# Kernel tuning notes

Hardware: AMD Instinct MI355X
Metric: run time of the kernel (lower is better)

The kernel has to match this reference:

```python
import jax, jax.numpy as jnp
import numpy as np

B, S, E, H = 4, 512, 512, 8
DH = E // H
HID = max(16, E // 4)  # sr_ratio=4
ALPHA = 0.1
EPS_SAFE = 0.05  # eps=1e-6 clamped to [0.05, 0.8]


def _xavier(k, shape):
    fan_out, fan_in = shape[0], shape[1]
    lim = (6.0 / (fan_in + fan_out)) ** 0.5
    return jax.random.uniform(k, shape, minval=-lim, maxval=lim, dtype=jnp.float32)


def setup_inputs() -> dict:
    key = jax.random.key(0)
    ks = jax.random.split(key, 8)
    return {
        "x": jax.random.normal(ks[0], (B, S, E), dtype=jnp.float32),
        "wq": _xavier(ks[1], (E, E)), "bq": jnp.zeros((E,), jnp.float32),
        "wk": _xavier(ks[2], (E, E)), "bk": jnp.zeros((E,), jnp.float32),
        "wv": _xavier(ks[3], (E, E)), "bv": jnp.zeros((E,), jnp.float32),
        "wo": _xavier(ks[4], (E, E)), "bo": jnp.zeros((E,), jnp.float32),
        # sr_conv1: Conv2d(1, HID, 1) -> weight [HID,1,1,1] == vector [HID]
        "w1": _xavier(ks[5], (HID, 1)).reshape(HID), "b1": jnp.zeros((HID,), jnp.float32),
        # sr_conv2: Conv2d(HID, 1, 1) -> weight [1,HID,1,1] == vector [HID]
        "w2": _xavier(ks[6], (1, HID)).reshape(HID), "b2": jnp.zeros((), jnp.float32),
    }


def _autopoietic_transform(scores, w1, b1, w2, b2):
    # scores: [B, H, S, S]
    scores = jnp.clip(jnp.nan_to_num(scores, nan=0.0, posinf=10.0, neginf=-10.0), -15.0, 15.0)
    mean_attn = scores.mean(axis=1)  # mean over heads -> [B, S, S]

    scaled = jnp.clip(jnp.clip(mean_attn, -8.0, 8.0) * EPS_SAFE, -10.0, 10.0)
    # conv1x1 (1 -> HID): broadcastmul; clamp + relu; conv1x1 (HID -> 1)
    hid = scaled[:, None, :, :] * w1[None, :, None, None] + b1[None, :, None, None]  # [B,HID,S,S]
    hid = jax.nn.relu(jnp.clip(hid, -5.0, 5.0))
    auto = jnp.einsum('bhij,h->bij', hid, w2) + b2  # [B,S,S]
    auto = jnp.clip(auto, -5.0, 5.0)

    # Taylor expansion with clamp, then sigmoid smoothing
    taylor = jnp.clip(1.0 + 0.05 * (auto * 50.0), 0.5, 1.5)
    sig = jax.nn.sigmoid(taylor)

    # fuzzy probability via entropy of softmax of mean attention
    p = jax.nn.softmax(jnp.clip(mean_attn, -10.0, 10.0), axis=-1)
    Hent = -p * jnp.log(p + 1e-6)
    Fm = jax.nn.softmax(3.0 * Hent, axis=-1)

    t = sig * Fm

    # energy (Frobenius-norm) balancing per batch
    e_o = jnp.sqrt((mean_attn ** 2).sum(axis=(1, 2))) + 1e-4
    e_t = jnp.sqrt((t ** 2).sum(axis=(1, 2))) + 1e-4
    gamma = jnp.clip(e_o / e_t, 0.8, 1.2)[:, None, None]
    t = gamma * t

    # dynamic std matching
    t_mean = t.mean(axis=(1, 2), keepdims=True)
    o_mean = mean_attn.mean(axis=(1, 2), keepdims=True)
    t_std = jnp.sqrt(jnp.clip(((t - t_mean) ** 2).mean(axis=(1, 2), keepdims=True), 0.01, None))
    o_std = jnp.sqrt(jnp.clip(((mean_attn - o_mean) ** 2).mean(axis=(1, 2), keepdims=True), 0.01, None))
    gdyn = jnp.clip(o_std / t_std, 0.8, 1.2)
    t = o_mean + gdyn * (t - t_mean)

    # residual blend of transformed map back into per-head scores (alpha=0.1), final clamp
    return jnp.clip(scores + ALPHA * t[:, None, :, :], -15.0, 15.0)


def reference(x, wq, bq, wk, bk, wv, bv, wo, bo, w1, b1, w2, b2):
    scaling = DH ** -0.5
    q = (jnp.einsum('bse,oe->bso', x, wq) + bq).reshape(B, S, H, DH).transpose(0, 2, 1, 3) * scaling
    k = (jnp.einsum('bse,oe->bso', x, wk) + bk).reshape(B, S, H, DH).transpose(0, 2, 1, 3)
    v = (jnp.einsum('bse,oe->bso', x, wv) + bv).reshape(B, S, H, DH).transpose(0, 2, 1, 3)
    scores = jnp.einsum('bhqd,bhkd->bhqk', q, k)  # [B,H,S,S]
    scores = _autopoietic_transform(scores, w1, b1, w2, b2)
    attn = jax.nn.softmax(scores, axis=-1)
    out = jnp.einsum('bhqk,bhkd->bhqd', attn, v).transpose(0, 2, 1, 3).reshape(B, S, E)
    return jnp.einsum('bse,oe->bso', out, wo) + bo
```

## Files before the change

### kernel.cpp

```cpp
#include <hip/hip_runtime.h>
#include <math.h>

#define BATCH 4
#define SEQ   512
#define EMB   512
#define NH    8
#define DHD   64
#define HIDN  128
#define ALPHA 0.1f
#define EPSS  0.05f

#define LUTN  2048
#define XMIN  (-0.4f)
#define XSTEP (0.8f / LUTN)

typedef __attribute__((ext_vector_type(8))) short  bf16x8;
typedef __attribute__((ext_vector_type(4))) float  f32x4;
#define MFMA(a,b,c) __builtin_amdgcn_mfma_f32_16x16x32_bf16((a),(b),(c),0,0,0)

__device__ __forceinline__ unsigned short f2bf(float f) {
    union { float f; unsigned u; } v; v.f = f;
    unsigned r = v.u + 0x7fffu + ((v.u >> 16) & 1u);
    return (unsigned short)(r >> 16);
}
__device__ __forceinline__ float bf2f(unsigned short h) {
    union { unsigned u; float f; } v; v.u = ((unsigned)h) << 16;
    return v.f;
}
__device__ __forceinline__ float f16tof(unsigned short h) {
    union { unsigned short s; _Float16 f; } v; v.s = h; return (float)v.f;
}
__device__ __forceinline__ unsigned short ftof16(float f) {
    union { unsigned short s; _Float16 f; } v; v.f = (_Float16)f; return v.s;
}

__device__ __forceinline__ void async_lds16(const unsigned short* g, unsigned short* l) {
    __builtin_amdgcn_global_load_lds(
        (const __attribute__((address_space(1))) void*)g,
        (__attribute__((address_space(3))) void*)l, 16, 0, 0);
}

template<int KS, int UN, int MT>
__device__ __forceinline__ void gemm_core64(
    const unsigned short* __restrict__ A, const unsigned short* __restrict__ B,
    int m0, int n0, unsigned short* sA, unsigned short* sB, f32x4 (&acc)[2][4])
{
    const int K = KS * 64;
    const int tid = threadIdx.x, w = tid >> 6, lane = tid & 63;
    const int quad = lane >> 4, r = lane & 15;
    const int wm = w >> 1, wn = w & 1;
    const int lrow = lane >> 3, lc = lane & 7;
    const int sc = lc ^ lrow;
    constexpr int AF = MT / 32;
    constexpr int NB = UN * 32 / 32;

    const unsigned short* ag[2]; unsigned short* dAu[2];
    #pragma unroll
    for (int c = 0; c < AF; c++) {
        const int rb = w * (8 * AF) + c * 8;
        ag[c]  = A + (long)(m0 + rb + lrow) * K + sc * 8;
        dAu[c] = sA + rb * 64;
    }
    const unsigned short* bg[4]; unsigned short* dBu[4];
    #pragma unroll
    for (int c = 0; c < NB; c++) {
        const int rb = w * (8 * NB) + c * 8;
        bg[c]  = B + (long)(n0 + rb + lrow) * K + sc * 8;
        dBu[c] = sB + rb * 64;
    }

    for (int s = 0; s < KS; s++) {
        const int k0 = s * 64;
        #pragma unroll
        for (int c = 0; c < AF; c++) async_lds16(ag[c] + k0, dAu[c]);
        #pragma unroll
        for (int c = 0; c < NB; c++) async_lds16(bg[c] + k0, dBu[c]);
        __syncthreads();
        #pragma unroll
        for (int kc = 0; kc < 2; kc++) {
            bf16x8 af[2], bfr[4];
            #pragma unroll
            for (int t = 0; t < AF; t++) {
                const int row = wm * (16 * AF) + t * 16 + r;
                af[t] = *(const bf16x8*)(sA + row * 64 + ((kc * 4 + quad) ^ (row & 7)) * 8);
            }
            #pragma unroll
            for (int u = 0; u < UN; u++) {
                const int row = wn * (16 * UN) + u * 16 + r;
                bfr[u] = *(const bf16x8*)(sB + row * 64 + ((kc * 4 + quad) ^ (row & 7)) * 8);
            }
            #pragma unroll
            for (int t = 0; t < AF; t++)
                #pragma unroll
                for (int u = 0; u < UN; u++)
                    acc[t][u] = MFMA(af[t], bfr[u], acc[t][u]);
        }
        __syncthreads();
    }
}

__global__ __launch_bounds__(256) void gemm_qkv(
    const unsigned short* __restrict__ x_ext, const unsigned short* __restrict__ w_ext,
    const float* __restrict__ bq, const float* __restrict__ bk, const float* __restrict__ bv,
    unsigned short* __restrict__ q_ext, unsigned short* __restrict__ k_ext,
    unsigned short* __restrict__ vT)
{
    __shared__ __align__(16) unsigned short sA[64 * 64];
    __shared__ __align__(16) unsigned short sB[64 * 64];
    __shared__ float sC[64 * 68];

    const int m0 = blockIdx.y * 64, n0 = blockIdx.x * 64;
    f32x4 acc[2][4] = {};
    gemm_core64<24, 2, 64>(x_ext, w_ext, m0, n0, sA, sB, acc);

    const int tid = threadIdx.x, w = tid >> 6, lane = tid & 63;
    const int quad = lane >> 4, r = lane & 15;
    const int wm = w >> 1, wn = w & 1;
    #pragma unroll
    for (int t = 0; t < 2; t++)
        #pragma unroll
        for (int u = 0; u < 2; u++)
            #pragma unroll
            for (int g = 0; g < 4; g++)
                sC[(wm * 32 + t * 16 + quad * 4 + g) * 68 + wn * 32 + u * 16 + r] = acc[t][u][g];
    __syncthreads();

    const int which = n0 >> 9;
    const int n0l = n0 & 511;
    const int h0 = n0l >> 6;
    const int b = m0 >> 9, s0 = m0 & 511;

    if (which < 2) {
        const float scl = (which == 0) ? 0.125f : 1.0f;
        const float* bias = (which == 0) ? bq : bk;
        unsigned* dst = (unsigned*)((which == 0) ? q_ext : k_ext);
        #pragma unroll
        for (int seg = 0; seg < 3; seg++) {
            const bool lo = (which == 0) ? (seg == 1) : (seg == 2);
            #pragma unroll
            for (int it = 0; it < 8; it++) {
                const int idx = it * 256 + tid;
                const int sl = idx >> 5;
                const int jc = idx & 31;
                const int nc = jc * 2;
                float v0 = (sC[sl * 68 + nc]     + bias[n0l + nc])     * scl;
                float v1 = (sC[sl * 68 + nc + 1] + bias[n0l + nc + 1]) * scl;
                unsigned short a0 = f2bf(v0), a1 = f2bf(v1);
                if (lo) { a0 = f2bf(v0 - bf2f(a0)); a1 = f2bf(v1 - bf2f(a1)); }
                const long orow = (long)(b * NH + h0) * SEQ + s0 + sl;
                dst[orow * 96 + seg * 32 + jc] = (unsigned)a0 | ((unsigned)a1 << 16);
            }
        }
    } else {
        unsigned* dst = (unsigned*)vT;
        #pragma unroll
        for (int it = 0; it < 8; it++) {
            const int idx = it * 256 + tid;
            const int d = idx >> 5;
            const int jc = idx & 31;
            const int sl = jc * 2;
            const float bvv = bv[n0l + d];
            const float v0 = sC[sl * 68 + d] + bvv;
            const float v1 = sC[(sl + 1) * 68 + d] + bvv;
            const long orow = (long)(b * NH + h0) * DHD + d;
            dst[orow * 256 + (s0 >> 1) + jc] = (unsigned)f2bf(v0) | ((unsigned)f2bf(v1) << 16);
        }
    }
}

__global__ __launch_bounds__(256) void gemm_scores(
    const unsigned short* __restrict__ q_ext, const unsigned short* __restrict__ k_ext,
    unsigned short* __restrict__ scoresH)
{
    __shared__ __align__(16) unsigned short sA[64 * 64];
    __shared__ __align__(16) unsigned short sB[128 * 64];
    const int z = blockIdx.z;
    const int m0 = blockIdx.y * 64, n0 = blockIdx.x * 128;
    f32x4 acc[2][4] = {};
    gemm_core64<3, 4, 64>(q_ext + (long)z * SEQ * 192, k_ext + (long)z * SEQ * 192,
                          m0, n0, sA, sB, acc);

    const int tid = threadIdx.x, w = tid >> 6, lane = tid & 63;
    const int quad = lane >> 4, r = lane & 15;
    const int wm = w >> 1, wn = w & 1;
    unsigned short* hC = sB;
    #pragma unroll
    for (int t = 0; t < 2; t++)
        #pragma unroll
        for (int u = 0; u < 4; u++)
            #pragma unroll
            for (int g = 0; g < 4; g++) {
                const int ml = wm * 32 + t * 16 + quad * 4 + g;
                const int nl = wn * 64 + u * 16 + r;
                hC[ml * 128 + nl] = ftof16(fminf(fmaxf(acc[t][u][g], -15.f), 15.f));
            }
    __syncthreads();
    #pragma unroll
    for (int it = 0; it < 4; it++) {
        const int id = it * 256 + tid;
        const int ml = id >> 4, ch = id & 15;
        *(uint4*)(scoresH + ((long)z * SEQ + m0 + ml) * SEQ + n0 + ch * 8) =
            *(const uint4*)(hC + ml * 128 + ch * 8);
    }
}

__global__ __launch_bounds__(256) void gemm_proj(
    const unsigned short* __restrict__ otmp, const unsigned short* __restrict__ woh,
    const float* __restrict__ bo, float* __restrict__ out)
{
    __shared__ __align__(16) unsigned short sA[32 * 64];
    __shared__ __align__(16) unsigned short sB[64 * 64];
    const int m0 = blockIdx.y * 32, n0 = blockIdx.x * 64;
    f32x4 acc[2][4] = {};
    gemm_core64<8, 2, 32>(otmp, woh, m0, n0, sA, sB, acc);
    const int tid = threadIdx.x, w = tid >> 6, lane = tid & 63;
    const int quad = lane >> 4, r = lane & 15;
    const int wm = w >> 1, wn = w & 1;
    #pragma unroll
    for (int u = 0; u < 2; u++)
        #pragma unroll
        for (int g = 0; g < 4; g++) {
            const int m = m0 + wm * 16 + quad * 4 + g;
            const int n = n0 + wn * 32 + u * 16 + r;
            out[(long)m * EMB + n] = acc[0][u][g] + bo[n];
        }
}

__device__ __forceinline__ float blockReduceSum(float v, float* sred) {
    #pragma unroll
    for (int o = 32; o > 0; o >>= 1) v += __shfl_down(v, o);
    __syncthreads();
    if ((threadIdx.x & 63) == 0) sred[threadIdx.x >> 6] = v;
    __syncthreads();
    return (sred[0] + sred[1]) + (sred[2] + sred[3]);
}
__device__ __forceinline__ float blockReduceMax(float v, float* sred) {
    #pragma unroll
    for (int o = 32; o > 0; o >>= 1) v = fmaxf(v, __shfl_down(v, o));
    __syncthreads();
    if ((threadIdx.x & 63) == 0) sred[threadIdx.x >> 6] = v;
    __syncthreads();
    return fmaxf(fmaxf(sred[0], sred[1]), fmaxf(sred[2], sred[3]));
}

__global__ __launch_bounds__(256) void prep_kernel(
    const float* __restrict__ x,
    const float* __restrict__ wq, const float* __restrict__ wk,
    const float* __restrict__ wv, const float* __restrict__ wo,
    const float* __restrict__ w1, const float* __restrict__ b1,
    const float* __restrict__ w2, const float* __restrict__ b2,
    unsigned short* __restrict__ x_ext, unsigned short* __restrict__ w_ext,
    unsigned short* __restrict__ woh, float* __restrict__ lut)
{
    const int blk = blockIdx.x;
    if (blk < 9) {
        const int i = blk * 256 + threadIdx.x;
        if (i > LUTN) return;
        const float xv = XMIN + i * XSTEP;
        float a = 0.f;
        for (int h = 0; h < HIDN; h++) {
            float hv = xv * w1[h] + b1[h];
            hv = fminf(fmaxf(hv, -5.f), 5.f);
            hv = fmaxf(hv, 0.f);
            a += hv * w2[h];
        }
        a += b2[0];
        a = fminf(fmaxf(a, -5.f), 5.f);
        const float taylor = fminf(fmaxf(1.f + 2.5f * a, 0.5f), 1.5f);
        lut[i] = 1.f / (1.f + expf(-taylor));
        return;
    }
    const int i = (blk - 9) * 256 + threadIdx.x;
    if (i < 1048576) {
        const int m = i >> 9, k = i & 511;
        const float v = x[i];
        const unsigned short h = f2bf(v), l = f2bf(v - bf2f(h));
        const long bb = (long)m * 1536 + k;
        x_ext[bb] = h; x_ext[bb + 512] = l; x_ext[bb + 1024] = h;
    } else if (i < 1835008) {
        const int j = i - 1048576;
        const int n = j >> 9, k = j & 511;
        const float v = (j < 262144) ? wq[j] : (j < 524288 ? wk[j - 262144] : wv[j - 524288]);
        const unsigned short h = f2bf(v), l = f2bf(v - bf2f(h));
        const long bb = (long)n * 1536 + k;
        w_ext[bb] = h; w_ext[bb + 512] = h; w_ext[bb + 1024] = l;
    } else {
        const int j = i - 1835008;
        woh[j] = f2bf(wo[j]);
    }
}

__global__ __launch_bounds__(256) void transform_kernel(
    const unsigned short* __restrict__ scoresH,
    const float* __restrict__ lut,
    unsigned short* __restrict__ t0H,
    float4* __restrict__ partials)
{
    const int rr = blockIdx.x;
    const int b = rr >> 9, i = rr & 511;
    const int tid = threadIdx.x;

    __shared__ float slut[LUTN + 1];
    __shared__ float sred[4];

    for (int u = tid; u <= LUTN; u += 256) slut[u] = lut[u];

    const unsigned* baseU =
        (const unsigned*)(scoresH + (((long)(b * NH)) * SEQ + i) * SEQ) + tid;
    float s0 = 0.f, s1 = 0.f;
    #pragma unroll
    for (int h = 0; h < NH; h++) {
        const unsigned pv = baseU[h * (SEQ * SEQ / 2)];
        s0 += f16tof((unsigned short)pv);
        s1 += f16tof((unsigned short)(pv >> 16));
    }
    float mv[2] = { s0 * 0.125f, s1 * 0.125f };
    __syncthreads();

    float sigv[2], mclip[2];
    float lmax = -1e30f;
    #pragma unroll
    for (int u = 0; u < 2; u++) {
        const float m = mv[u];
        const float x = fminf(fmaxf(m, -8.f), 8.f) * EPSS;
        float t = (x - XMIN) * (1.0f / XSTEP);
        int idx = (int)t;
        idx = idx < 0 ? 0 : (idx > LUTN - 1 ? LUTN - 1 : idx);
        const float frac = t - (float)idx;
        const float l0 = slut[idx], l1 = slut[idx + 1];
        sigv[u] = l0 + frac * (l1 - l0);
        const float mc = fminf(fmaxf(m, -10.f), 10.f);
        mclip[u] = mc;
        lmax = fmaxf(lmax, mc);
    }

    const float rmax = blockReduceMax(lmax, sred);
    float ex[2], lsum = 0.f;
    #pragma unroll
    for (int u = 0; u < 2; u++) { ex[u] = expf(mclip[u] - rmax); lsum += ex[u]; }
    const float rsum = blockReduceSum(lsum, sred);
    const float inv = 1.f / rsum;

    float hent[2], lmax2 = -1e30f;
    #pragma unroll
    for (int u = 0; u < 2; u++) {
        const float p = ex[u] * inv;
        const float he = -p * logf(p + 1e-6f);
        hent[u] = 3.f * he;
        lmax2 = fmaxf(lmax2, hent[u]);
    }
    const float rmax2 = blockReduceMax(lmax2, sred);
    float ex2[2], lsum2 = 0.f;
    #pragma unroll
    for (int u = 0; u < 2; u++) { ex2[u] = expf(hent[u] - rmax2); lsum2 += ex2[u]; }
    const float rsum2 = blockReduceSum(lsum2, sred);
    const float inv2 = 1.f / rsum2;

    float tv[2];
    #pragma unroll
    for (int u = 0; u < 2; u++) tv[u] = sigv[u] * (ex2[u] * inv2);
    ((unsigned*)t0H)[((long)b * SEQ + i) * (SEQ / 2) + tid] =
        (unsigned)ftof16(tv[0]) | ((unsigned)ftof16(tv[1]) << 16);

    float s_m  = blockReduceSum(mv[0] + mv[1], sred);
    float s_m2 = blockReduceSum(mv[0] * mv[0] + mv[1] * mv[1], sred);
    float s_t  = blockReduceSum(tv[0] + tv[1], sred);
    float s_t2 = blockReduceSum(tv[0] * tv[0] + tv[1] * tv[1], sred);
    if (tid == 0) partials[rr] = make_float4(s_m, s_m2, s_t, s_t2);
}

__global__ __launch_bounds__(256) void softmax_attnv(
    const unsigned short* __restrict__ scoresH,
    const unsigned short* __restrict__ t0H,
    const float4* __restrict__ partials,
    const unsigned short* __restrict__ vT,
    unsigned short* __restrict__ otmp)
{
    __shared__ __align__(16) unsigned short attnS[32 * 520];
    __shared__ __align__(16) unsigned short sB[64 * 64];
    __shared__ float sC[32 * 66];
    __shared__ float sred[4];

    const int m0 = blockIdx.x * 32;
    const int z  = blockIdx.y;
    const int b  = z >> 3, h = z & 7;
    const int tid = threadIdx.x, wv = tid >> 6, lane = tid & 63;

    const float4 p0 = partials[b * SEQ + tid];
    const float4 p1 = partials[b * SEQ + tid + 256];
    float sm  = blockReduceSum(p0.x + p1.x, sred);
    float sm2 = blockReduceSum(p0.y + p1.y, sred);
    float st  = blockReduceSum(p0.z + p1.z, sred);
    float st2 = blockReduceSum(p0.w + p1.w, sred);
    const float n = (float)SEQ * (float)SEQ;
    const float gamma = fminf(fmaxf((sqrtf(sm2) + 1e-4f) / (sqrtf(st2) + 1e-4f), 0.8f), 1.2f);
    const float o_mean = sm / n, t0m = st / n;
    const float o_std = sqrtf(fmaxf(fmaxf(sm2 / n - o_mean * o_mean, 0.f), 0.01f));
    const float t_std = sqrtf(fmaxf(gamma * gamma * fmaxf(st2 / n - t0m * t0m, 0.f), 0.01f));
    const float gdyn = fminf(fmaxf(o_std / t_std, 0.8f), 1.2f);
    const float c1 = gdyn * gamma;
    const float c0 = o_mean - c1 * t0m;

    const int j0 = lane * 8;
    for (int it = 0; it < 8; it++) {
        const int rowl = it * 4 + wv;
        const bf16x8 sr = *(const bf16x8*)(scoresH + ((long)z * SEQ + m0 + rowl) * SEQ + j0);
        const bf16x8 tr = *(const bf16x8*)(t0H + ((long)b * SEQ + m0 + rowl) * SEQ + j0);
        float sv[8];
        float lmax = -1e30f;
        #pragma unroll
        for (int u = 0; u < 8; u++) {
            float s = f16tof((unsigned short)sr[u])
                    + ALPHA * (c0 + c1 * f16tof((unsigned short)tr[u]));
            s = fminf(fmaxf(s, -15.f), 15.f);
            sv[u] = s;
            lmax = fmaxf(lmax, s);
        }
        #pragma unroll
        for (int o = 32; o > 0; o >>= 1) lmax = fmaxf(lmax, __shfl_down(lmax, o));
        lmax = __shfl(lmax, 0);
        float lsum = 0.f;
        #pragma unroll
        for (int u = 0; u < 8; u++) { sv[u] = expf(sv[u] - lmax); lsum += sv[u]; }
        #pragma unroll
        for (int o = 32; o > 0; o >>= 1) lsum += __shfl_down(lsum, o);
        lsum = __shfl(lsum, 0);
        const float inv = 1.f / lsum;
        bf16x8 pk;
        #pragma unroll
        for (int u = 0; u < 8; u++) pk[u] = (short)f2bf(sv[u] * inv);
        *(bf16x8*)(attnS + rowl * 520 + j0) = pk;
    }
    __syncthreads();

    const int quad = lane >> 4, r = lane & 15;
    const int wm = wv >> 1, wn = wv & 1;
    const int lrow = lane >> 3, lc = lane & 7;
    const int sc = lc ^ lrow;
    const unsigned short* bg0 = vT + (long)z * DHD * SEQ + (long)(wv * 16 + lrow) * SEQ + sc * 8;
    const unsigned short* bg1 = bg0 + 8 * SEQ;
    unsigned short* dB0 = sB + (wv * 16) * 64;
    unsigned short* dB1 = sB + (wv * 16 + 8) * 64;
    f32x4 acc[2] = {};
    for (int s = 0; s < 8; s++) {
        const int k0 = s * 64;
        async_lds16(bg0 + k0, dB0);
        async_lds16(bg1 + k0, dB1);
        __syncthreads();
        #pragma unroll
        for (int kc = 0; kc < 2; kc++) {
            const bf16x8 a = *(const bf16x8*)(attnS + (wm * 16 + r) * 520 + k0 + kc * 32 + quad * 8);
            #pragma unroll
            for (int u = 0; u < 2; u++) {
                const int row = wn * 32 + u * 16 + r;
                const bf16x8 bb = *(const bf16x8*)(sB + row * 64 + ((kc * 4 + quad) ^ (row & 7)) * 8);
                acc[u] = MFMA(a, bb, acc[u]);
            }
        }
        __syncthreads();
    }

    #pragma unroll
    for (int u = 0; u < 2; u++)
        #pragma unroll
        for (int g = 0; g < 4; g++)
            sC[(wm * 16 + quad * 4 + g) * 66 + wn * 32 + u * 16 + r] = acc[u][g];
    __syncthreads();
    unsigned* dst = (unsigned*)otmp;
    #pragma unroll
    for (int it = 0; it < 4; it++) {
        const int idx = it * 256 + tid;
        const int sr2 = idx >> 5, jc = idx & 31;
        const float v0 = sC[sr2 * 66 + jc * 2], v1 = sC[sr2 * 66 + jc * 2 + 1];
        dst[((long)(b * SEQ + m0 + sr2)) * 256 + h * 32 + jc] =
            (unsigned)f2bf(v0) | ((unsigned)f2bf(v1) << 16);
    }
}

extern "C" void kernel_launch(void* const* d_in, const int* in_sizes, int n_in,
                              void* d_out, int out_size, void* d_ws, size_t ws_size,
                              hipStream_t stream) {
    const float* x  = (const float*)d_in[0];
    const float* wq = (const float*)d_in[1];
    const float* bq = (const float*)d_in[2];
    const float* wk = (const float*)d_in[3];
    const float* bk = (const float*)d_in[4];
    const float* wv = (const float*)d_in[5];
    const float* bv = (const float*)d_in[6];
    const float* wo = (const float*)d_in[7];
    const float* bo = (const float*)d_in[8];
    const float* w1 = (const float*)d_in[9];
    const float* b1 = (const float*)d_in[10];
    const float* w2 = (const float*)d_in[11];
    const float* b2 = (const float*)d_in[12];
    float* out = (float*)d_out;

    char* wsb = (char*)d_ws;
    unsigned short* scoresH = (unsigned short*)wsb;
    unsigned short* t0H     = scoresH + 8388608;
    float4* partials = (float4*)(t0H + 1048576);
    float*  lutbuf   = (float*)(partials + 2048);
    unsigned short* u16 = (unsigned short*)(wsb + (20u << 20));
    unsigned short* x_ext = u16;
    unsigned short* w_ext = x_ext + 3145728;
    unsigned short* q_ext = w_ext + 2359296;
    unsigned short* k_ext = q_ext + 3145728;
    unsigned short* vT    = k_ext + 3145728;
    unsigned short* otmp  = vT + 1048576;
    unsigned short* woh   = otmp + 1048576;

    prep_kernel<<<dim3(9 + 8192), dim3(256), 0, stream>>>(
        x, wq, wk, wv, wo, w1, b1, w2, b2, x_ext, w_ext, woh, lutbuf);

    gemm_qkv<<<dim3(24, 32), dim3(256), 0, stream>>>(
        x_ext, w_ext, bq, bk, bv, q_ext, k_ext, vT);

    gemm_scores<<<dim3(4, 8, 32), dim3(256), 0, stream>>>(q_ext, k_ext, scoresH);

    transform_kernel<<<dim3(BATCH * SEQ), dim3(256), 0, stream>>>(
        scoresH, lutbuf, t0H, partials);

    softmax_attnv<<<dim3(16, 32), dim3(256), 0, stream>>>(
        scoresH, t0H, partials, vT, otmp);

    gemm_proj<<<dim3(8, 64), dim3(256), 0, stream>>>(otmp, woh, bo, out);
}
```

Baseline: 148.6 us.

## Enlarge QKV GEMM tiles to 128x128 and preload whole V in attnV kernel

The QKV projection GEMM moves from 64x64 to 128x128 output tiles, with each wave computing a 64x64 sub-tile. The epilogue is split into two 64-row halves so the staging buffer stays bounded. The softmax+attnV kernel now handles 64 query rows per block and loads the whole V^T head slice into LDS asynchronously at kernel start, overlapping that load with the softmax and dropping the per-K-step barriers. The cost is fewer blocks (192 and 256), which may leave CUs idle on a 256-CU part, plus much larger LDS per block and lower occupancy.

```diff
diff --git a/kernel.cpp b/kernel.cpp
--- a/kernel.cpp
+++ b/kernel.cpp
@@ -52,7 +52,7 @@
     const int lrow = lane >> 3, lc = lane & 7;
     const int sc = lc ^ lrow;
     constexpr int AF = MT / 32;
-    constexpr int NB = UN * 32 / 32;
+    constexpr int NB = UN;
 
     const unsigned short* ag[2]; unsigned short* dAu[2];
     #pragma unroll
@@ -105,66 +105,115 @@
     unsigned short* __restrict__ q_ext, unsigned short* __restrict__ k_ext,
     unsigned short* __restrict__ vT)
 {
-    __shared__ __align__(16) unsigned short sA[64 * 64];
-    __shared__ __align__(16) unsigned short sB[64 * 64];
-    __shared__ float sC[64 * 68];
-
-    const int m0 = blockIdx.y * 64, n0 = blockIdx.x * 64;
-    f32x4 acc[2][4] = {};
-    gemm_core64<24, 2, 64>(x_ext, w_ext, m0, n0, sA, sB, acc);
-
+    __shared__ __align__(16) unsigned short sA[128 * 64];
+    __shared__ __align__(16) unsigned short sB[128 * 64];
+    __shared__ float sC[64 * 132];
+
+    const int m0 = blockIdx.y * 128, n0 = blockIdx.x * 128;
     const int tid = threadIdx.x, w = tid >> 6, lane = tid & 63;
     const int quad = lane >> 4, r = lane & 15;
     const int wm = w >> 1, wn = w & 1;
-    #pragma unroll
-    for (int t = 0; t < 2; t++)
-        #pragma unroll
-        for (int u = 0; u < 2; u++)
-            #pragma unroll
-            for (int g = 0; g < 4; g++)
-                sC[(wm * 32 + t * 16 + quad * 4 + g) * 68 + wn * 32 + u * 16 + r] = acc[t][u][g];
-    __syncthreads();
+    const int lrow = lane >> 3, lc = lane & 7;
+    const int sc = lc ^ lrow;
+
+    f32x4 acc[4][4] = {};
+    const unsigned short* ag[4]; const unsigned short* bg[4];
+    unsigned short *dA[4], *dB[4];
+    #pragma unroll
+    for (int c = 0; c < 4; c++) {
+        const int rb = w * 32 + c * 8;
+        ag[c] = x_ext + (long)(m0 + rb + lrow) * 1536 + sc * 8;
+        bg[c] = w_ext + (long)(n0 + rb + lrow) * 1536 + sc * 8;
+        dA[c] = sA + rb * 64;
+        dB[c] = sB + rb * 64;
+    }
+
+    for (int s = 0; s < 24; s++) {
+        const int k0 = s * 64;
+        #pragma unroll
+        for (int c = 0; c < 4; c++) { async_lds16(ag[c] + k0, dA[c]); async_lds16(bg[c] + k0, dB[c]); }
+        __syncthreads();
+        #pragma unroll
+        for (int kc = 0; kc < 2; kc++) {
+            bf16x8 af[4], bfr[4];
+            #pragma unroll
+            for (int t = 0; t < 4; t++) {
+                const int row = wm * 64 + t * 16 + r;
+                af[t] = *(const bf16x8*)(sA + row * 64 + ((kc * 4 + quad) ^ (row & 7)) * 8);
+            }
+            #pragma unroll
+            for (int u = 0; u < 4; u++) {
+                const int row = wn * 64 + u * 16 + r;
+                bfr[u] = *(const bf16x8*)(sB + row * 64 + ((kc * 4 + quad) ^ (row & 7)) * 8);
+            }
+            #pragma unroll
+            for (int t = 0; t < 4; t++)
+                #pragma unroll
+                for (int u = 0; u < 4; u++)
+                    acc[t][u] = MFMA(af[t], bfr[u], acc[t][u]);
+        }
+        __syncthreads();
+    }
 
     const int which = n0 >> 9;
     const int n0l = n0 & 511;
-    const int h0 = n0l >> 6;
-    const int b = m0 >> 9, s0 = m0 & 511;
-
-    if (which < 2) {
-        const float scl = (which == 0) ? 0.125f : 1.0f;
-        const float* bias = (which == 0) ? bq : bk;
-        unsigned* dst = (unsigned*)((which == 0) ? q_ext : k_ext);
-        #pragma unroll
-        for (int seg = 0; seg < 3; seg++) {
-            const bool lo = (which == 0) ? (seg == 1) : (seg == 2);
-            #pragma unroll
-            for (int it = 0; it < 8; it++) {
+    const int b = m0 >> 9;
+
+    #pragma unroll
+    for (int p = 0; p < 2; p++) {
+        if (wm == p) {
+            #pragma unroll
+            for (int t = 0; t < 4; t++)
+                #pragma unroll
+                for (int u = 0; u < 4; u++)
+                    #pragma unroll
+                    for (int g = 0; g < 4; g++)
+                        sC[(t * 16 + quad * 4 + g) * 132 + wn * 64 + u * 16 + r] = acc[t][u][g];
+        }
+        __syncthreads();
+        const int s0r = (m0 & 511) + p * 64;
+        if (which < 2) {
+            const float scl = (which == 0) ? 0.125f : 1.0f;
+            const float* bias = (which == 0) ? bq : bk;
+            unsigned* dst = (unsigned*)((which == 0) ? q_ext : k_ext);
+            #pragma unroll
+            for (int seg = 0; seg < 3; seg++) {
+                const bool lo = (which == 0) ? (seg == 1) : (seg == 2);
+                #pragma unroll
+                for (int it = 0; it < 16; it++) {
+                    const int idx = it * 256 + tid;
+                    const int sl = idx >> 6;
+                    const int jc = idx & 63;
+                    const int nc = jc * 2;
+                    const int n2 = n0l + nc;
+                    const int h = n2 >> 6, d = n2 & 63;
+                    float v0 = (sC[sl * 132 + nc]     + bias[n2])     * scl;
+                    float v1 = (sC[sl * 132 + nc + 1] + bias[n2 + 1]) * scl;
+                    unsigned short a0 = f2bf(v0), a1 = f2bf(v1);
+                    if (lo) { a0 = f2bf(v0 - bf2f(a0)); a1 = f2bf(v1 - bf2f(a1)); }
+                    const long orow = (long)(b * NH + h) * SEQ + s0r + sl;
+                    dst[orow * 96 + seg * 32 + (d >> 1)] = (unsigned)a0 | ((unsigned)a1 << 16);
+                }
+            }
+        } else {
+            unsigned* dst = (unsigned*)vT;
+            #pragma unroll
+            for (int it = 0; it < 16; it++) {
                 const int idx = it * 256 + tid;
-                const int sl = idx >> 5;
+                const int dcol = idx >> 5;
                 const int jc = idx & 31;
-                const int nc = jc * 2;
-                float v0 = (sC[sl * 68 + nc]     + bias[n0l + nc])     * scl;
-                float v1 = (sC[sl * 68 + nc + 1] + bias[n0l + nc + 1]) * scl;
-                unsigned short a0 = f2bf(v0), a1 = f2bf(v1);
-                if (lo) { a0 = f2bf(v0 - bf2f(a0)); a1 = f2bf(v1 - bf2f(a1)); }
-                const long orow = (long)(b * NH + h0) * SEQ + s0 + sl;
-                dst[orow * 96 + seg * 32 + jc] = (unsigned)a0 | ((unsigned)a1 << 16);
-            }
-        }
-    } else {
-        unsigned* dst = (unsigned*)vT;
-        #pragma unroll
-        for (int it = 0; it < 8; it++) {
-            const int idx = it * 256 + tid;
-            const int d = idx >> 5;
-            const int jc = idx & 31;
-            const int sl = jc * 2;
-            const float bvv = bv[n0l + d];
-            const float v0 = sC[sl * 68 + d] + bvv;
-            const float v1 = sC[(sl + 1) * 68 + d] + bvv;
-            const long orow = (long)(b * NH + h0) * DHD + d;
-            dst[orow * 256 + (s0 >> 1) + jc] = (unsigned)f2bf(v0) | ((unsigned)f2bf(v1) << 16);
-        }
+                const int sl = jc * 2;
+                const int n2 = n0l + dcol;
+                const int h = n2 >> 6, d = n2 & 63;
+                const float bvv = bv[n2];
+                const float v0 = sC[sl * 132 + dcol] + bvv;
+                const float v1 = sC[(sl + 1) * 132 + dcol] + bvv;
+                const long orow = (long)(b * NH + h) * DHD + d;
+                dst[orow * 256 + ((m0 & 511) >> 1) + p * 32 + jc] =
+                    (unsigned)f2bf(v0) | ((unsigned)f2bf(v1) << 16);
+            }
+        }
+        __syncthreads();
     }
 }
 
@@ -376,15 +425,21 @@
     const unsigned short* __restrict__ vT,
     unsigned short* __restrict__ otmp)
 {
-    __shared__ __align__(16) unsigned short attnS[32 * 520];
-    __shared__ __align__(16) unsigned short sB[64 * 64];
-    __shared__ float sC[32 * 66];
+    __shared__ __align__(16) unsigned short attnS[64 * 520];
+    __shared__ __align__(16) unsigned short vL[64 * 520];
     __shared__ float sred[4];
 
-    const int m0 = blockIdx.x * 32;
+    const int m0 = blockIdx.x * 64;
     const int z  = blockIdx.y;
     const int b  = z >> 3, h = z & 7;
     const int tid = threadIdx.x, wv = tid >> 6, lane = tid & 63;
+
+    const unsigned short* vg = vT + (long)z * DHD * SEQ + lane * 8;
+    #pragma unroll
+    for (int c = 0; c < 16; c++) {
+        const int d = c * 4 + wv;
+        async_lds16(vg + d * SEQ, vL + d * 520);
+    }
 
     const float4 p0 = partials[b * SEQ + tid];
     const float4 p1 = partials[b * SEQ + tid + 256];
@@ -402,7 +457,7 @@
     const float c0 = o_mean - c1 * t0m;
 
     const int j0 = lane * 8;
-    for (int it = 0; it < 8; it++) {
+    for (int it = 0; it < 16; it++) {
         const int rowl = it * 4 + wv;
         const bf16x8 sr = *(const bf16x8*)(scoresH + ((long)z * SEQ + m0 + rowl) * SEQ + j0);
         const bf16x8 tr = *(const bf16x8*)(t0H + ((long)b * SEQ + m0 + rowl) * SEQ + j0);
@@ -434,41 +489,28 @@
     __syncthreads();
 
     const int quad = lane >> 4, r = lane & 15;
-    const int wm = wv >> 1, wn = wv & 1;
-    const int lrow = lane >> 3, lc = lane & 7;
-    const int sc = lc ^ lrow;
-    const unsigned short* bg0 = vT + (long)z * DHD * SEQ + (long)(wv * 16 + lrow) * SEQ + sc * 8;
-    const unsigned short* bg1 = bg0 + 8 * SEQ;
-    unsigned short* dB0 = sB + (wv * 16) * 64;
-    unsigned short* dB1 = sB + (wv * 16 + 8) * 64;
-    f32x4 acc[2] = {};
-    for (int s = 0; s < 8; s++) {
-        const int k0 = s * 64;
-        async_lds16(bg0 + k0, dB0);
-        async_lds16(bg1 + k0, dB1);
-        __syncthreads();
-        #pragma unroll
-        for (int kc = 0; kc < 2; kc++) {
-            const bf16x8 a = *(const bf16x8*)(attnS + (wm * 16 + r) * 520 + k0 + kc * 32 + quad * 8);
-            #pragma unroll
-            for (int u = 0; u < 2; u++) {
-                const int row = wn * 32 + u * 16 + r;
-                const bf16x8 bb = *(const bf16x8*)(sB + row * 64 + ((kc * 4 + quad) ^ (row & 7)) * 8);
-                acc[u] = MFMA(a, bb, acc[u]);
-            }
-        }
-        __syncthreads();
-    }
-
-    #pragma unroll
-    for (int u = 0; u < 2; u++)
+    f32x4 acc[4] = {};
+    #pragma unroll
+    for (int kc = 0; kc < 16; kc++) {
+        const bf16x8 a = *(const bf16x8*)(attnS + (wv * 16 + r) * 520 + kc * 32 + quad * 8);
+        #pragma unroll
+        for (int u = 0; u < 4; u++) {
+            const bf16x8 bb = *(const bf16x8*)(vL + (u * 16 + r) * 520 + kc * 32 + quad * 8);
+            acc[u] = MFMA(a, bb, acc[u]);
+        }
+    }
+    __syncthreads();
+
+    float* sC = (float*)attnS;
+    #pragma unroll
+    for (int u = 0; u < 4; u++)
         #pragma unroll
         for (int g = 0; g < 4; g++)
-            sC[(wm * 16 + quad * 4 + g) * 66 + wn * 32 + u * 16 + r] = acc[u][g];
+            sC[(wv * 16 + quad * 4 + g) * 66 + u * 16 + r] = acc[u][g];
     __syncthreads();
     unsigned* dst = (unsigned*)otmp;
     #pragma unroll
-    for (int it = 0; it < 4; it++) {
+    for (int it = 0; it < 8; it++) {
         const int idx = it * 256 + tid;
         const int sr2 = idx >> 5, jc = idx & 31;
         const float v0 = sC[sr2 * 66 + jc * 2], v1 = sC[sr2 * 66 + jc * 2 + 1];
@@ -512,7 +554,7 @@
     prep_kernel<<<dim3(9 + 8192), dim3(256), 0, stream>>>(
         x, wq, wk, wv, wo, w1, b1, w2, b2, x_ext, w_ext, woh, lutbuf);
 
-    gemm_qkv<<<dim3(24, 32), dim3(256), 0, stream>>>(
+    gemm_qkv<<<dim3(12, 16), dim3(256), 0, stream>>>(
         x_ext, w_ext, bq, bk, bv, q_ext, k_ext, vT);
 
     gemm_scores<<<dim3(4, 8, 32), dim3(256), 0, stream>>>(q_ext, k_ext, scoresH);
@@ -520,7 +562,7 @@
     transform_kernel<<<dim3(BATCH * SEQ), dim3(256), 0, stream>>>(
         scoresH, lutbuf, t0H, partials);
 
-    softmax_attnv<<<dim3(16, 32), dim3(256), 0, stream>>>(
+    softmax_attnv<<<dim3(8, 32), dim3(256), 0, stream>>>(
         scoresH, t0H, partials, vT, otmp);
 
     gemm_proj<<<dim3(8, 64), dim3(256), 0, stream>>>(otmp, woh, bo, out);
```

Measured after the change: 169.6 us. 1.14x slower.
